# Kernel tuning notes

Hardware: AMD Instinct MI355X
Metric: run time of the kernel (lower is better)

The kernel has to match this reference:

```python
import jax, jax.numpy as jnp
import numpy as np

EMBED_DIM = 1024
SHIFT = 0.0

def setup_inputs() -> dict:
    key = jax.random.key(0)
    k1, k2, k3 = jax.random.split(key, 3)
    inputs = jax.random.normal(k1, (4, 2048, EMBED_DIM), dtype=jnp.float32)
    rotation_params = jax.random.normal(k2, (EMBED_DIM, EMBED_DIM), dtype=jnp.float32)
    entangle_params = jax.random.normal(k3, (EMBED_DIM, EMBED_DIM), dtype=jnp.float32)
    return {"inputs": inputs, "rotation_params": rotation_params, "entangle_params": entangle_params}

def reference(inputs, rotation_params, entangle_params):
    # inputs: (b, s, d)
    d = inputs.shape[-1]
    query = jnp.einsum('bsd,de->bse', inputs, rotation_params)
    key = jnp.einsum('bsd,de->bse', inputs, entangle_params)
    scores = jax.nn.softmax(jnp.einsum('bqd,bkd->bqk', query, key) / np.sqrt(d), axis=-1)
    out = jnp.einsum('bqk,bkd->bqd', scores, inputs)
    return jax.nn.sigmoid(out + SHIFT)
```

## Files before the change

### kernel.cpp

```cpp
#include <hip/hip_runtime.h>
#include <hip/hip_bf16.h>
#include <math.h>


using u16 = unsigned short;
using short8 = __attribute__((ext_vector_type(8))) short;
using f32x4  = __attribute__((ext_vector_type(4))) float;

#define MFB(a, b, c) __builtin_amdgcn_mfma_f32_16x16x32_bf16((a), (b), (c), 0, 0, 0)

__device__ static inline u16 f2bf(float f) {
    union { __hip_bfloat16 h; u16 u; } cv; cv.h = __float2bfloat16(f); return cv.u;
}
__device__ static inline float bf2f(u16 u) {
    union { __hip_bfloat16 h; u16 u; } cv; cv.u = u; return __bfloat162float(cv.h);
}
__device__ static inline void split2(float v, u16& h, u16& l) {
    h = f2bf(v);
    l = f2bf(v - bf2f(h));
}

__device__ static inline void gload16(const u16* g, u16* l) {
    __builtin_amdgcn_global_load_lds(
        (const __attribute__((address_space(1))) void*)g,
        (__attribute__((address_space(3))) void*)l, 16, 0, 0);
}

__device__ static inline short8 ldfrag(const u16* sm, int row, int g) {
    const int off = row * 32 + ((g ^ ((row >> 1) & 3)) << 3);
    return *reinterpret_cast<const short8*>(sm + off);
}

enum { EP_F32 = 0, EP_HILO = 1, EP_SIG = 2 };

template<int EPI, bool TRIPLE>
__global__ __launch_bounds__(256)
void gemm_split(const u16* __restrict__ Ahi, const u16* __restrict__ Alo,
                const u16* __restrict__ Bhi, const u16* __restrict__ Blo,
                float* __restrict__ Cf, u16* __restrict__ Chi, u16* __restrict__ Clo,
                int K, int lda, int ldb, int ldc,
                long sA, long sB, long sC, float alpha)
{
    const int z = blockIdx.z;
    Ahi += z * sA;
    Bhi += z * sB;
    if (TRIPLE) { Alo += z * sA; Blo += z * sB; }
    if (EPI == EP_HILO) { Chi += z * sC; Clo += z * sC; }
    else                { Cf  += z * sC; }

    constexpr int BUFSZ  = TRIPLE ? 16384 : 8192;
    constexpr int OFF_BH = TRIPLE ? 8192 : 4096;
    __shared__ __align__(16) u16 smem[2 * BUFSZ];

    const int t = threadIdx.x;
    const int wave = t >> 6, lane = t & 63;
    const int row0 = blockIdx.y * 128, col0 = blockIdx.x * 128;

    const int rr = t >> 2, cc = t & 3;
    const int gg = cc ^ ((rr >> 1) & 3);
    const u16* gAh = Ahi + (long)(row0 + rr) * lda + gg * 8;
    const u16* gBh = Bhi + (long)(col0 + rr) * ldb + gg * 8;
    const u16* gAl = TRIPLE ? (Alo + (long)(row0 + rr) * lda + gg * 8) : nullptr;
    const u16* gBl = TRIPLE ? (Blo + (long)(col0 + rr) * ldb + gg * 8) : nullptr;
    const long a2 = (long)64 * lda, b2 = (long)64 * ldb;

    f32x4 acc[4][4];
    #pragma unroll
    for (int m = 0; m < 4; m++)
        #pragma unroll
        for (int n = 0; n < 4; n++)
            acc[m][n] = (f32x4){0.f, 0.f, 0.f, 0.f};

    const int lr = lane & 15, lg = lane >> 4;
    const int wm = (wave >> 1) * 64, wn = (wave & 1) * 64;
    const int NT = K >> 5;

    {
        u16* d = smem + t * 8;
        gload16(gAh,      d);
        gload16(gAh + a2, d + 2048);
        gload16(gBh,      d + OFF_BH);
        gload16(gBh + b2, d + OFF_BH + 2048);
        if (TRIPLE) {
            gload16(gAl,      d + 4096);
            gload16(gAl + a2, d + 4096 + 2048);
            gload16(gBl,      d + 12288);
            gload16(gBl + b2, d + 12288 + 2048);
        }
    }

    for (int tk = 0; tk < NT; ++tk) {
        __syncthreads();
        const u16* sb = smem + (tk & 1) * BUFSZ;
        if (tk + 1 < NT) {
            const int kn = (tk + 1) << 5;
            u16* d = smem + ((tk + 1) & 1) * BUFSZ + t * 8;
            gload16(gAh + kn,      d);
            gload16(gAh + kn + a2, d + 2048);
            gload16(gBh + kn,      d + OFF_BH);
            gload16(gBh + kn + b2, d + OFF_BH + 2048);
            if (TRIPLE) {
                gload16(gAl + kn,      d + 4096);
                gload16(gAl + kn + a2, d + 4096 + 2048);
                gload16(gBl + kn,      d + 12288);
                gload16(gBl + kn + b2, d + 12288 + 2048);
            }
        }
        const u16* sAh = sb;
        const u16* sAl = sb + 4096;
        const u16* sBh = sb + OFF_BH;
        const u16* sBl = sb + 12288;

        short8 bh[4], bl[4];
        #pragma unroll
        for (int n = 0; n < 4; n++) {
            bh[n] = ldfrag(sBh, wn + n * 16 + lr, lg);
            if (TRIPLE) bl[n] = ldfrag(sBl, wn + n * 16 + lr, lg);
        }
        #pragma unroll
        for (int m = 0; m < 4; m++) {
            const short8 ah = ldfrag(sAh, wm + m * 16 + lr, lg);
            short8 al;
            if (TRIPLE) al = ldfrag(sAl, wm + m * 16 + lr, lg);
            #pragma unroll
            for (int n = 0; n < 4; n++) {
                acc[m][n] = MFB(ah, bh[n], acc[m][n]);
                if (TRIPLE) {
                    acc[m][n] = MFB(ah, bl[n], acc[m][n]);
                    acc[m][n] = MFB(al, bh[n], acc[m][n]);
                }
            }
        }
    }

    #pragma unroll
    for (int m = 0; m < 4; m++) {
        #pragma unroll
        for (int n = 0; n < 4; n++) {
            #pragma unroll
            for (int r = 0; r < 4; r++) {
                const int grow = row0 + wm + m * 16 + lg * 4 + r;
                const int gcol = col0 + wn + n * 16 + lr;
                const float v = alpha * acc[m][n][r];
                const long o = (long)grow * ldc + gcol;
                if (EPI == EP_F32) {
                    Cf[o] = v;
                } else if (EPI == EP_SIG) {
                    Cf[o] = 1.0f / (1.0f + __expf(-v));
                } else {
                    u16 h, l; split2(v, h, l);
                    Chi[o] = h; Clo[o] = l;
                }
            }
        }
    }
}

__global__ __launch_bounds__(512)
void gemm_triple_256(const u16* __restrict__ Ahi, const u16* __restrict__ Alo,
                     const u16* __restrict__ Bhi, const u16* __restrict__ Blo,
                     float* __restrict__ Cf,
                     int K, int lda, int ldb, int ldc,
                     long sA, long sB, long sC, float alpha)
{
    const int z = blockIdx.z;
    Ahi += z * sA; Alo += z * sA;
    Bhi += z * sB; Blo += z * sB;
    Cf  += z * sC;

    __shared__ __align__(16) u16 smem[65536];

    const int t = threadIdx.x;
    const int wave = t >> 6, lane = t & 63;
    const int lr = lane & 15, lg = lane >> 4;

    const int u = blockIdx.x + 8 * blockIdx.y;
    const int reg = u & 7, j = u >> 3;
    const int bx = 2 * (reg & 3) + (j & 1);
    const int by = 4 * (reg >> 2) + (j >> 1);
    const int row0 = by * 256, col0 = bx * 256;
    const int wm = (wave >> 2) * 128, wn = (wave & 3) * 64;

    const int srow = t >> 2;
    const int sg = (t & 3) ^ ((srow >> 1) & 3);
    const u16* gAh = Ahi + (long)(row0 + srow) * lda + sg * 8;
    const u16* gAl = Alo + (long)(row0 + srow) * lda + sg * 8;
    const u16* gBh = Bhi + (long)(col0 + srow) * ldb + sg * 8;
    const u16* gBl = Blo + (long)(col0 + srow) * ldb + sg * 8;
    const long a2 = (long)128 * lda, b2 = (long)128 * ldb;

    f32x4 acc[8][4];
    #pragma unroll
    for (int m = 0; m < 8; m++)
        #pragma unroll
        for (int n = 0; n < 4; n++)
            acc[m][n] = (f32x4){0.f, 0.f, 0.f, 0.f};

    const int NT = K >> 5;

    {
        u16* d = smem + t * 8;
        gload16(gAh,      d);          gload16(gAh + a2, d + 4096);
        gload16(gAl,      d + 8192);   gload16(gAl + a2, d + 12288);
        gload16(gBh,      d + 16384);  gload16(gBh + b2, d + 20480);
        gload16(gBl,      d + 24576);  gload16(gBl + b2, d + 28672);
    }

    for (int tk = 0; tk < NT; ++tk) {
        __syncthreads();
        const u16* sb = smem + (tk & 1) * 32768;
        if (tk + 1 < NT) {
            const int kn = (tk + 1) << 5;
            u16* d = smem + ((tk + 1) & 1) * 32768 + t * 8;
            gload16(gAh + kn,      d);          gload16(gAh + kn + a2, d + 4096);
            gload16(gAl + kn,      d + 8192);   gload16(gAl + kn + a2, d + 12288);
            gload16(gBh + kn,      d + 16384);  gload16(gBh + kn + b2, d + 20480);
            gload16(gBl + kn,      d + 24576);  gload16(gBl + kn + b2, d + 28672);
        }
        const u16* sAh = sb;
        const u16* sAl = sb + 8192;
        const u16* sBh = sb + 16384;
        const u16* sBl = sb + 24576;

        short8 bh[4], bl[4];
        #pragma unroll
        for (int n = 0; n < 4; n++) {
            bh[n] = ldfrag(sBh, wn + n * 16 + lr, lg);
            bl[n] = ldfrag(sBl, wn + n * 16 + lr, lg);
        }
        #pragma unroll
        for (int m = 0; m < 8; m++) {
            const short8 ah = ldfrag(sAh, wm + m * 16 + lr, lg);
            const short8 al = ldfrag(sAl, wm + m * 16 + lr, lg);
            #pragma unroll
            for (int n = 0; n < 4; n++) {
                acc[m][n] = MFB(ah, bh[n], acc[m][n]);
                acc[m][n] = MFB(ah, bl[n], acc[m][n]);
                acc[m][n] = MFB(al, bh[n], acc[m][n]);
            }
        }
    }

    #pragma unroll
    for (int m = 0; m < 8; m++) {
        #pragma unroll
        for (int n = 0; n < 4; n++) {
            #pragma unroll
            for (int r = 0; r < 4; r++) {
                const int grow = row0 + wm + m * 16 + lg * 4 + r;
                const int gcol = col0 + wn + n * 16 + lr;
                Cf[(long)grow * ldc + gcol] = alpha * acc[m][n][r];
            }
        }
    }
}

__global__ __launch_bounds__(256)
void split_rm3(const float* __restrict__ in0, u16* __restrict__ hi0, u16* __restrict__ lo0, long n0,
               const float* __restrict__ in1, u16* __restrict__ hi1, u16* __restrict__ lo1, long n1,
               const float* __restrict__ in2, u16* __restrict__ hi2, u16* __restrict__ lo2)
{
    long i = ((long)blockIdx.x * 256 + threadIdx.x) * 4;
    const float* in; u16 *hi, *lo;
    if (i < n0)           { in = in0; hi = hi0; lo = lo0; }
    else if (i < n0 + n1) { i -= n0; in = in1; hi = hi1; lo = lo1; }
    else                  { i -= n0 + n1; in = in2; hi = hi2; lo = lo2; }
    const float4 v = *reinterpret_cast<const float4*>(in + i);
    ushort4 h, l;
    split2(v.x, h.x, l.x);
    split2(v.y, h.y, l.y);
    split2(v.z, h.z, l.z);
    split2(v.w, h.w, l.w);
    *reinterpret_cast<ushort4*>(hi + i) = h;
    *reinterpret_cast<ushort4*>(lo + i) = l;
}

__global__ __launch_bounds__(256)
void reduce4_split(const float* __restrict__ p, u16* __restrict__ hi, u16* __restrict__ lo,
                   long n)
{
    const long i = ((long)blockIdx.x * 256 + threadIdx.x) * 4;
    const float4 a = *reinterpret_cast<const float4*>(p + i);
    const float4 b = *reinterpret_cast<const float4*>(p + n + i);
    const float4 c = *reinterpret_cast<const float4*>(p + 2 * n + i);
    const float4 d = *reinterpret_cast<const float4*>(p + 3 * n + i);
    ushort4 h, l;
    split2((a.x + b.x) + (c.x + d.x), h.x, l.x);
    split2((a.y + b.y) + (c.y + d.y), h.y, l.y);
    split2((a.z + b.z) + (c.z + d.z), h.z, l.z);
    split2((a.w + b.w) + (c.w + d.w), h.w, l.w);
    *reinterpret_cast<ushort4*>(hi + i) = h;
    *reinterpret_cast<ushort4*>(lo + i) = l;
}

template<bool HILO>
__global__ __launch_bounds__(256)
void split_tr(const float* __restrict__ in, u16* __restrict__ hi, u16* __restrict__ lo,
              int R, int C, long sIn, long sOut)
{
    in += (long)blockIdx.z * sIn;
    hi += (long)blockIdx.z * sOut;
    if (HILO) lo += (long)blockIdx.z * sOut;

    __shared__ float tile[32][33];
    const int tx = threadIdx.x & 31, ty = threadIdx.x >> 5;
    const int r0 = blockIdx.y * 32, c0 = blockIdx.x * 32;

    #pragma unroll
    for (int j = 0; j < 4; j++)
        tile[ty * 4 + j][tx] = in[(long)(r0 + ty * 4 + j) * C + c0 + tx];
    __syncthreads();

    #pragma unroll
    for (int j = 0; j < 4; j++) {
        const int oc = ty * 4 + j;
        const float v = tile[tx][oc];
        u16 h, l; split2(v, h, l);
        const long o = (long)(c0 + oc) * R + r0 + tx;
        hi[o] = h;
        if (HILO) lo[o] = l;
    }
}

__global__ __launch_bounds__(256)
void softmax_hi(const float* __restrict__ S, u16* __restrict__ hi)
{
    const int NC = 2048;
    const long base = (long)blockIdx.x * NC;
    const float* p = S + base;
    const int tid = threadIdx.x;

    float4 v0 = reinterpret_cast<const float4*>(p)[tid];
    float4 v1 = reinterpret_cast<const float4*>(p)[tid + 256];

    float m = fmaxf(fmaxf(fmaxf(v0.x, v0.y), fmaxf(v0.z, v0.w)),
                    fmaxf(fmaxf(v1.x, v1.y), fmaxf(v1.z, v1.w)));
    #pragma unroll
    for (int off = 1; off < 64; off <<= 1)
        m = fmaxf(m, __shfl_xor(m, off));

    __shared__ float redm[4];
    __shared__ float reds[4];
    const int wave = tid >> 6, lane = tid & 63;
    if (lane == 0) redm[wave] = m;
    __syncthreads();
    m = fmaxf(fmaxf(redm[0], redm[1]), fmaxf(redm[2], redm[3]));

    v0.x = __expf(v0.x - m); v0.y = __expf(v0.y - m);
    v0.z = __expf(v0.z - m); v0.w = __expf(v0.w - m);
    v1.x = __expf(v1.x - m); v1.y = __expf(v1.y - m);
    v1.z = __expf(v1.z - m); v1.w = __expf(v1.w - m);

    float s = (v0.x + v0.y + v0.z + v0.w) + (v1.x + v1.y + v1.z + v1.w);
    #pragma unroll
    for (int off = 1; off < 64; off <<= 1)
        s += __shfl_xor(s, off);
    if (lane == 0) reds[wave] = s;
    __syncthreads();
    s = (reds[0] + reds[1]) + (reds[2] + reds[3]);

    const float inv = 1.0f / s;
    ushort4 h0, h1;
    h0.x = f2bf(v0.x * inv); h0.y = f2bf(v0.y * inv);
    h0.z = f2bf(v0.z * inv); h0.w = f2bf(v0.w * inv);
    h1.x = f2bf(v1.x * inv); h1.y = f2bf(v1.y * inv);
    h1.z = f2bf(v1.z * inv); h1.w = f2bf(v1.w * inv);

    reinterpret_cast<ushort4*>(hi + base)[tid]       = h0;
    reinterpret_cast<ushort4*>(hi + base)[tid + 256] = h1;
}

extern "C" void kernel_launch(void* const* d_in, const int* in_sizes, int n_in,
                              void* d_out, int out_size, void* d_ws, size_t ws_size,
                              hipStream_t stream)
{
    (void)in_sizes; (void)n_in; (void)out_size; (void)ws_size;
    const float* X = (const float*)d_in[0];
    const float* R = (const float*)d_in[1];
    const float* E = (const float*)d_in[2];
    float* out = (float*)d_out;

    const int B = 4, SQ = 2048, D = 1024;
    const long NDX = (long)B * SQ * D;
    const long DD  = (long)D * D;
    const long SS  = (long)B * SQ * SQ;
    const long M16 = 8388608;

    u16* wsu = (u16*)d_ws;
    u16* Xhi  = wsu;
    u16* Xlo  = Xhi + NDX;
    u16* Rhi  = wsu + 2 * M16;
    u16* Rlo  = Rhi + DD;
    u16* Ehi  = Rlo + DD;
    u16* Elo  = Ehi + DD;
    u16* Yhi  = wsu + 2 * M16;
    u16* Ylo  = Yhi + NDX;
    u16* Shi  = wsu + 2 * M16;
    u16* Xthi = wsu;
    float* Wpart = (float*)(wsu + 4 * M16);
    u16* Wthi = wsu + 5 * M16;
    u16* Wtlo = Wthi + DD;
    float* Sf = (float*)(wsu + 4 * M16);

    dim3 thr(256);

    split_rm3<<<dim3((unsigned)((NDX + 2 * DD) / 1024)), thr, 0, stream>>>(
        X, Xhi, Xlo, NDX, R, Rhi, Rlo, DD, E, Ehi, Elo);

    gemm_split<EP_F32, true><<<dim3(D / 128, D / 128, 4), thr, 0, stream>>>(
        Ehi, Elo, Rhi, Rlo, Wpart, nullptr, nullptr,
        256, D, D, D, 256, 256, DD, 1.0f);
    reduce4_split<<<dim3((unsigned)(DD / 1024)), thr, 0, stream>>>(Wpart, Wthi, Wtlo, DD);

    gemm_split<EP_HILO, true><<<dim3(D / 128, (B * SQ) / 128, 1), thr, 0, stream>>>(
        Xhi, Xlo, Wthi, Wtlo, nullptr, Yhi, Ylo,
        D, D, D, D, 0, 0, 0, 1.0f);

    gemm_triple_256<<<dim3(SQ / 256, SQ / 256, B), dim3(512), 0, stream>>>(
        Yhi, Ylo, Xhi, Xlo, Sf,
        D, D, D, SQ,
        (long)SQ * D, (long)SQ * D, (long)SQ * SQ, 0.03125f);

    softmax_hi<<<dim3(B * SQ), thr, 0, stream>>>(Sf, Shi);

    split_tr<false><<<dim3(D / 32, SQ / 32, B), thr, 0, stream>>>(
        X, Xthi, nullptr, SQ, D, (long)SQ * D, (long)SQ * D);

    gemm_split<EP_SIG, false><<<dim3(D / 128, SQ / 128, B), thr, 0, stream>>>(
        Shi, nullptr, Xthi, nullptr, out, nullptr, nullptr,
        SQ, SQ, SQ, D,
        (long)SQ * SQ, (long)SQ * D, (long)SQ * D, 1.0f);
}
```

Measured before the change: 245.8 us.

## Split A/B staging with explicit vmcnt waits and barriers in split GEMMs

Reorganizes shared memory into separate A and B double-buffered slots and replaces the single __syncthreads per k-step with fine-grained s_waitcnt vmcnt plus raw s_barrier. B for the next tile is prefetched first, then A after B fragments are read, so loads overlap compute more and the full vmcnt(0) drain implied by __syncthreads is avoided. The 256-tile kernel also raises wave priority around the MFMA loop. This relies on the hand-counted vmcnt values matching how the compiler orders outstanding loads, which is fragile.

After: 245.6 us. About the same (-0.1%).

```diff
diff --git a/kernel.cpp b/kernel.cpp
--- a/kernel.cpp
+++ b/kernel.cpp
@@ -48,9 +48,8 @@
     if (EPI == EP_HILO) { Chi += z * sC; Clo += z * sC; }
     else                { Cf  += z * sC; }
 
-    constexpr int BUFSZ  = TRIPLE ? 16384 : 8192;
-    constexpr int OFF_BH = TRIPLE ? 8192 : 4096;
-    __shared__ __align__(16) u16 smem[2 * BUFSZ];
+    constexpr int SLOT = TRIPLE ? 8192 : 4096;
+    __shared__ __align__(16) u16 smem[4 * SLOT];
 
     const int t = threadIdx.x;
     const int wave = t >> 6, lane = t & 63;
@@ -64,6 +63,25 @@
     const u16* gBl = TRIPLE ? (Blo + (long)(col0 + rr) * ldb + gg * 8) : nullptr;
     const long a2 = (long)64 * lda, b2 = (long)64 * ldb;
 
+    auto STAGE_B = [&](int s, int kk) {
+        u16* d = smem + s * SLOT + t * 8;
+        gload16(gBh + kk,      d);
+        gload16(gBh + kk + b2, d + 2048);
+        if (TRIPLE) {
+            gload16(gBl + kk,      d + 4096);
+            gload16(gBl + kk + b2, d + 6144);
+        }
+    };
+    auto STAGE_A = [&](int s, int kk) {
+        u16* d = smem + 2 * SLOT + s * SLOT + t * 8;
+        gload16(gAh + kk,      d);
+        gload16(gAh + kk + a2, d + 2048);
+        if (TRIPLE) {
+            gload16(gAl + kk,      d + 4096);
+            gload16(gAl + kk + a2, d + 6144);
+        }
+    };
+
     f32x4 acc[4][4];
     #pragma unroll
     for (int m = 0; m < 4; m++)
@@ -75,48 +93,37 @@
     const int wm = (wave >> 1) * 64, wn = (wave & 1) * 64;
     const int NT = K >> 5;
 
-    {
-        u16* d = smem + t * 8;
-        gload16(gAh,      d);
-        gload16(gAh + a2, d + 2048);
-        gload16(gBh,      d + OFF_BH);
-        gload16(gBh + b2, d + OFF_BH + 2048);
-        if (TRIPLE) {
-            gload16(gAl,      d + 4096);
-            gload16(gAl + a2, d + 4096 + 2048);
-            gload16(gBl,      d + 12288);
-            gload16(gBl + b2, d + 12288 + 2048);
-        }
-    }
+    STAGE_B(0, 0);
+    STAGE_A(0, 0);
 
     for (int tk = 0; tk < NT; ++tk) {
-        __syncthreads();
-        const u16* sb = smem + (tk & 1) * BUFSZ;
-        if (tk + 1 < NT) {
-            const int kn = (tk + 1) << 5;
-            u16* d = smem + ((tk + 1) & 1) * BUFSZ + t * 8;
-            gload16(gAh + kn,      d);
-            gload16(gAh + kn + a2, d + 2048);
-            gload16(gBh + kn,      d + OFF_BH);
-            gload16(gBh + kn + b2, d + OFF_BH + 2048);
-            if (TRIPLE) {
-                gload16(gAl + kn,      d + 4096);
-                gload16(gAl + kn + a2, d + 4096 + 2048);
-                gload16(gBl + kn,      d + 12288);
-                gload16(gBl + kn + b2, d + 12288 + 2048);
-            }
-        }
-        const u16* sAh = sb;
-        const u16* sAl = sb + 4096;
-        const u16* sBh = sb + OFF_BH;
-        const u16* sBl = sb + 12288;
-
+        const int cur = tk & 1;
+        if (TRIPLE) asm volatile("s_waitcnt vmcnt(4) lgkmcnt(0)" ::: "memory");
+        else        asm volatile("s_waitcnt vmcnt(2) lgkmcnt(0)" ::: "memory");
+        __builtin_amdgcn_s_barrier();
+        const bool pf = (tk + 1 < NT);
+        if (pf) STAGE_B(cur ^ 1, (tk + 1) << 5);
+
+        const u16* sBh = smem + cur * SLOT;
+        const u16* sBl = sBh + 4096;
         short8 bh[4], bl[4];
         #pragma unroll
         for (int n = 0; n < 4; n++) {
             bh[n] = ldfrag(sBh, wn + n * 16 + lr, lg);
             if (TRIPLE) bl[n] = ldfrag(sBl, wn + n * 16 + lr, lg);
         }
+
+        if (pf) {
+            if (TRIPLE) asm volatile("s_waitcnt vmcnt(4)" ::: "memory");
+            else        asm volatile("s_waitcnt vmcnt(2)" ::: "memory");
+        } else {
+            asm volatile("s_waitcnt vmcnt(0)" ::: "memory");
+        }
+        __builtin_amdgcn_s_barrier();
+        if (pf) STAGE_A(cur ^ 1, (tk + 1) << 5);
+
+        const u16* sAh = smem + 2 * SLOT + cur * SLOT;
+        const u16* sAl = sAh + 4096;
         #pragma unroll
         for (int m = 0; m < 4; m++) {
             const short8 ah = ldfrag(sAh, wm + m * 16 + lr, lg);
@@ -189,6 +196,21 @@
     const u16* gBl = Blo + (long)(col0 + srow) * ldb + sg * 8;
     const long a2 = (long)128 * lda, b2 = (long)128 * ldb;
 
+    auto STAGE_B = [&](int s, int kk) {
+        u16* d = smem + s * 16384 + t * 8;
+        gload16(gBh + kk,      d);
+        gload16(gBh + kk + b2, d + 4096);
+        gload16(gBl + kk,      d + 8192);
+        gload16(gBl + kk + b2, d + 12288);
+    };
+    auto STAGE_A = [&](int s, int kk) {
+        u16* d = smem + 32768 + s * 16384 + t * 8;
+        gload16(gAh + kk,      d);
+        gload16(gAh + kk + a2, d + 4096);
+        gload16(gAl + kk,      d + 8192);
+        gload16(gAl + kk + a2, d + 12288);
+    };
+
     f32x4 acc[8][4];
     #pragma unroll
     for (int m = 0; m < 8; m++)
@@ -198,36 +220,33 @@
 
     const int NT = K >> 5;
 
-    {
-        u16* d = smem + t * 8;
-        gload16(gAh,      d);          gload16(gAh + a2, d + 4096);
-        gload16(gAl,      d + 8192);   gload16(gAl + a2, d + 12288);
-        gload16(gBh,      d + 16384);  gload16(gBh + b2, d + 20480);
-        gload16(gBl,      d + 24576);  gload16(gBl + b2, d + 28672);
-    }
+    STAGE_B(0, 0);
+    STAGE_A(0, 0);
 
     for (int tk = 0; tk < NT; ++tk) {
-        __syncthreads();
-        const u16* sb = smem + (tk & 1) * 32768;
-        if (tk + 1 < NT) {
-            const int kn = (tk + 1) << 5;
-            u16* d = smem + ((tk + 1) & 1) * 32768 + t * 8;
-            gload16(gAh + kn,      d);          gload16(gAh + kn + a2, d + 4096);
-            gload16(gAl + kn,      d + 8192);   gload16(gAl + kn + a2, d + 12288);
-            gload16(gBh + kn,      d + 16384);  gload16(gBh + kn + b2, d + 20480);
-            gload16(gBl + kn,      d + 24576);  gload16(gBl + kn + b2, d + 28672);
-        }
-        const u16* sAh = sb;
-        const u16* sAl = sb + 8192;
-        const u16* sBh = sb + 16384;
-        const u16* sBl = sb + 24576;
-
+        const int cur = tk & 1;
+        asm volatile("s_waitcnt vmcnt(4) lgkmcnt(0)" ::: "memory");
+        __builtin_amdgcn_s_barrier();
+        const bool pf = (tk + 1 < NT);
+        if (pf) STAGE_B(cur ^ 1, (tk + 1) << 5);
+
+        const u16* sBh = smem + cur * 16384;
+        const u16* sBl = sBh + 8192;
         short8 bh[4], bl[4];
         #pragma unroll
         for (int n = 0; n < 4; n++) {
             bh[n] = ldfrag(sBh, wn + n * 16 + lr, lg);
             bl[n] = ldfrag(sBl, wn + n * 16 + lr, lg);
         }
+
+        if (pf) asm volatile("s_waitcnt vmcnt(4)" ::: "memory");
+        else    asm volatile("s_waitcnt vmcnt(0)" ::: "memory");
+        __builtin_amdgcn_s_barrier();
+        if (pf) STAGE_A(cur ^ 1, (tk + 1) << 5);
+
+        const u16* sAh = smem + 32768 + cur * 16384;
+        const u16* sAl = sAh + 8192;
+        __builtin_amdgcn_s_setprio(1);
         #pragma unroll
         for (int m = 0; m < 8; m++) {
             const short8 ah = ldfrag(sAh, wm + m * 16 + lr, lg);
@@ -239,6 +258,7 @@
                 acc[m][n] = MFB(al, bh[n], acc[m][n]);
             }
         }
+        __builtin_amdgcn_s_setprio(0);
     }
 
     #pragma unroll
```
